# Kernel optimization log

Measured on AMD Instinct MI355X. Metric: run time of the kernel, lower is better.

## Reference

```python
import jax, jax.numpy as jnp
import numpy as np

P = 16        # patch size
SIM = 0.3     # similarity threshold (forward default arg `sim`)
STY_STD = 1000.0


def patchify(imgs):
    # (N,3,H,W) -> (N, h*w, p*p*3)
    N, C, H, W = imgs.shape
    h, w = H // P, W // P
    x = imgs.reshape(N, C, h, P, w, P)
    x = jnp.einsum('nchpwq->nhwpqc', x)
    return x.reshape(N, h * w, P * P * C)


def setup_inputs() -> dict:
    key = jax.random.key(0)
    k1, k2, k3, k4 = jax.random.split(key, 4)
    N, L, D = 2, 196, 768
    x = jax.random.normal(k1, (N, L + 1, D), dtype=jnp.float32)
    imgs = jax.random.normal(k2, (N, 3, 224, 224), dtype=jnp.float32)
    # torch trunc_normal_(std=1000, a=-2, b=2) == truncated normal on [-2,2]
    learnable_sty = (jax.random.truncated_normal(
        k3, -2.0 / STY_STD, 2.0 / STY_STD, (N, L, L, 1), dtype=jnp.float32) * STY_STD)
    noise = jax.random.normal(k4, (N, L, L, 1), dtype=jnp.float32)
    return {"x": x, "imgs": imgs, "learnable_sty": learnable_sty, "noise": noise}


def reference(x, imgs, learnable_sty, noise):
    imgs = patchify(imgs)                                   # (N, L, 768)
    cls_tokens, x = x[:, :1], x[:, 1:]
    N, L, D = x.shape

    # per-patch normalization (torch.var default is unbiased -> ddof=1)
    mean = imgs.mean(axis=-1, keepdims=True)
    var = jnp.var(imgs, axis=-1, keepdims=True, ddof=1)
    imgs_n = (imgs - mean) / jnp.sqrt(var + 1e-6)
    nrm = jnp.linalg.norm(imgs_n, axis=-1)                  # (N, L)
    Sim = jnp.einsum('aik,ajk->aij', imgs_n, imgs_n) / (nrm[:, :, None] * nrm[:, None, :])

    M0 = jnp.triu((Sim > SIM).astype(jnp.float32))          # (N, L, L), binary
    rows = jnp.arange(L)

    def body(i, M):
        # original loop breaks when sum == N*L; we freeze M once that holds
        done = M.sum() == N * L
        mask = (M[:, i, :] == 0).astype(M.dtype)            # (N, L)
        # rows <= i unchanged (M*M == M for binary), rows > i masked
        upd = jnp.where(rows[None, :, None] > i, M * mask[:, None, :], M)
        return jnp.where(done, M, upd)

    M = jax.lax.fori_loop(0, L - 1, body, M0)

    # decompose: phase (con) keeps grad, amplitude (sty) is detached
    fft = jnp.fft.fftn(x, axes=(-1,))
    con, sty = jnp.angle(fft), jnp.abs(fft)
    sty_d = jax.lax.stop_gradient(sty)

    avg_sum = (M[..., None] * sty_d[:, None, :, :]).sum(axis=2)   # (N, L, D)
    sty_mask = (avg_sum > 0).astype(jnp.float32)                   # (N, L, D)
    num = M.sum(axis=2)[..., None]                                 # (N, L, 1)
    avg = avg_sum / jnp.clip(num, 1e-7, None)                      # (N, L, D)
    std = jnp.sqrt(
        (M[..., None] * (sty_d[:, None, :, :] - avg[:, :, None, :]) ** 2).sum(axis=2)
        / jnp.clip(num, 1e-7, None))                               # (N, L, D)

    sty_para = sty_mask[:, None, :, :] * learnable_sty             # (N, L, L, D)
    sty_para = sty_para / jnp.clip(sty_para.sum(axis=2, keepdims=True), 1e-7, None)
    various = noise * std[:, None, :, :] + avg[:, None, :, :]      # (N, L, L, D)
    sum_sty = (sty_para * various).sum(axis=2)                     # (N, L, D)

    # compose: ifft(amp * e^{i phase}), torch .float() keeps the real part
    out = jnp.real(jnp.fft.ifftn(sum_sty * jnp.exp(1j * con), axes=(-1,))).astype(jnp.float32)
    return jnp.concatenate((cls_tokens, out), axis=1)
```

## Files before the change

kernel.cpp:

```cpp
#include <hip/hip_runtime.h>
#include <math.h>

typedef unsigned long long u64;

#define NBATCH 2
#define LTOK 196
#define DDIM 768
#define NROWS (NBATCH*LTOK)
#define NLD (NBATCH*LTOK*DDIM)

#define PI_F 3.14159265358979323846f
#define S3 0.86602540378443864676f

__device__ __forceinline__ void fft_butterfly(float* re, float* im,
                                              const float2* T,
                                              int tau, int s, int half) {
  int sub = tau >> 7;
  int b = tau & 127;
  int j = b & (half - 1);
  int p0 = (sub << 8) + ((b >> (s - 1)) << s) + j;
  int p1 = p0 + half;
  float2 w = T[j << (8 - s)];
  float xr = re[p1], xi = im[p1];
  float tr = w.x * xr - w.y * xi;
  float ti = w.x * xi + w.y * xr;
  float ur = re[p0], ui = im[p0];
  re[p0] = ur + tr; im[p0] = ui + ti;
  re[p1] = ur - tr; im[p1] = ui - ti;
}

__device__ __forceinline__ void fft_stages(float* re, float* im,
                                           const float2* T, int t) {
#pragma unroll
  for (int s = 1; s <= 8; s++) {
    int half = 1 << (s - 1);
    fft_butterfly(re, im, T, t, s, half);
    if (t < 128) fft_butterfly(re, im, T, t + 256, s, half);
    __syncthreads();
  }
}

__global__ __launch_bounds__(256) void k_pre(const float* __restrict__ imgs,
                                             const float* __restrict__ x,
                                             float* __restrict__ uT,
                                             float* __restrict__ sty,
                                             float* __restrict__ phre,
                                             float* __restrict__ phim) {
  int t = threadIdx.x;
  if (blockIdx.x < NROWS) {
    int blk = blockIdx.x;
    int a = blk / LTOK, l = blk - a * LTOK;
    int hh = l / 14, ww = l - hh * 14;
    float loc[3];
    double s = 0.0, sq = 0.0;
#pragma unroll
    for (int e = 0; e < 3; e++) {
      int d = t + (e << 8);
      int p = d / 48, r = d - p * 48;
      int q2 = r / 3, c = r - q2 * 3;
      float val = imgs[((size_t)(a * 3 + c) * 224 + (hh * 16 + p)) * 224 + (ww * 16 + q2)];
      loc[e] = val;
      s += (double)val;
      sq += (double)val * (double)val;
    }
#pragma unroll
    for (int o = 32; o > 0; o >>= 1) { s += __shfl_down(s, o); sq += __shfl_down(sq, o); }
    __shared__ double rs[4], rq[4];
    __shared__ float sh_mu, sh_sc;
    if ((t & 63) == 0) { rs[t >> 6] = s; rq[t >> 6] = sq; }
    __syncthreads();
    if (t == 0) {
      double S = rs[0] + rs[1] + rs[2] + rs[3];
      double Q = rq[0] + rq[1] + rq[2] + rq[3];
      double mean = S / 768.0;
      double ss = Q - S * S / 768.0;
      if (ss < 1e-30) ss = 1e-30;
      sh_mu = (float)mean;
      sh_sc = (float)(1.0 / sqrt(ss));
    }
    __syncthreads();
    float mu = sh_mu, sc = sh_sc;
    int col = a * LTOK + l;
#pragma unroll
    for (int e = 0; e < 3; e++) {
      int d = t + (e << 8);
      uT[(size_t)d * NROWS + col] = (loc[e] - mu) * sc;
    }
  } else {
    int blk = blockIdx.x - NROWS;
    int a = blk / LTOK, i = blk - a * LTOK;
    __shared__ float re[768], im[768];
    __shared__ float2 t256[128];
    if (t < 128) {
      float sn, cs;
      __sincosf(-2.0f * PI_F * (float)t / 256.0f, &sn, &cs);
      t256[t] = make_float2(cs, sn);
    }
    size_t row = ((size_t)a * (LTOK + 1) + 1 + i) * DDIM;
#pragma unroll
    for (int e = 0; e < 3; e++) {
      int d = t + (e << 8);
      int m = d / 3, r = d - 3 * m;
      int p = (r << 8) + (__brev((unsigned)m) >> 24);
      re[p] = x[row + d];
      im[p] = 0.f;
    }
    __syncthreads();
    fft_stages(re, im, t256, t);
    float a0r = re[t],       a0i = im[t];
    float a1r = re[256 + t], a1i = im[256 + t];
    float a2r = re[512 + t], a2i = im[512 + t];
    float sn, cs;
    __sincosf(-2.0f * PI_F * (float)t / 768.0f, &sn, &cs);
    float2 w1 = make_float2(cs, sn);
    float2 w2 = make_float2(cs * cs - sn * sn, 2.f * cs * sn);
    float b1r = a1r * w1.x - a1i * w1.y, b1i = a1r * w1.y + a1i * w1.x;
    float b2r = a2r * w2.x - a2i * w2.y, b2i = a2r * w2.y + a2i * w2.x;
    float Xr[3], Xi[3];
    Xr[0] = a0r + b1r + b2r;
    Xi[0] = a0i + b1i + b2i;
    Xr[1] = a0r + (-0.5f * b1r + S3 * b1i) + (-0.5f * b2r - S3 * b2i);
    Xi[1] = a0i + (-0.5f * b1i - S3 * b1r) + (-0.5f * b2i + S3 * b2r);
    Xr[2] = a0r + (-0.5f * b1r - S3 * b1i) + (-0.5f * b2r + S3 * b2i);
    Xi[2] = a0i + (-0.5f * b1i + S3 * b1r) + (-0.5f * b2i - S3 * b2r);
    size_t ob = ((size_t)a * LTOK + i) * DDIM + t;
#pragma unroll
    for (int s = 0; s < 3; s++) {
      float mag = sqrtf(Xr[s] * Xr[s] + Xi[s] * Xi[s]);
      size_t o = ob + (s << 8);
      sty[o] = mag;
      if (mag > 0.f) { phre[o] = Xr[s] / mag; phim[o] = Xi[s] / mag; }
      else           { phre[o] = 1.f;         phim[o] = 0.f;         }
    }
  }
}

__global__ __launch_bounds__(256) void k_sim(const float* __restrict__ uT,
                                             u64* __restrict__ Mb) {
  int blk = blockIdx.x;
  int a = blk / LTOK, i = blk - a * LTOK;
  __shared__ float ui[768];
  __shared__ u64 mask[4];
  int t = threadIdx.x;
  if (t < 4) mask[t] = 0ull;
  int coli = a * LTOK + i;
#pragma unroll
  for (int e = 0; e < 3; e++) {
    int d = t + (e << 8);
    ui[d] = uT[(size_t)d * NROWS + coli];
  }
  __syncthreads();
  int j = i + t;
  if (j < LTOK) {
    const float* col = uT + (a * LTOK + j);
    float dot = 0.f;
#pragma unroll 8
    for (int d = 0; d < 768; d++) dot += ui[d] * col[(size_t)d * NROWS];
    if (dot > 0.3f) atomicOr(&mask[j >> 6], 1ull << (j & 63));
  }
  __syncthreads();
  if (t < 4) Mb[((size_t)a * LTOK + i) * 4 + t] = mask[t];
}

__global__ __launch_bounds__(256) void k_greedy(u64* __restrict__ Mb) {
  __shared__ u64 Ml[NROWS * 4];
  __shared__ int red[4];
  __shared__ int Sdone;
  int t = threadIdx.x;
  for (int w = t; w < NROWS * 4; w += 256) Ml[w] = Mb[w];
  __syncthreads();
  for (int i = 0; i < LTOK - 1; i++) {
    int s = 0;
    for (int w = t; w < NROWS * 4; w += 256) s += __popcll(Ml[w]);
#pragma unroll
    for (int o = 32; o > 0; o >>= 1) s += __shfl_down(s, o);
    if ((t & 63) == 0) red[t >> 6] = s;
    __syncthreads();
    if (t == 0) Sdone = ((red[0] + red[1] + red[2] + red[3]) == NROWS) ? 1 : 0;
    __syncthreads();
    if (Sdone) break;
    for (int w = t; w < NROWS * 4; w += 256) {
      int a = w / (LTOK * 4);
      int rem = w - a * (LTOK * 4);
      int r = rem >> 2, wi = rem & 3;
      if (r > i) Ml[w] &= ~Ml[(a * LTOK + i) * 4 + wi];
    }
    __syncthreads();
  }
  for (int w = t; w < NROWS * 4; w += 256) Mb[w] = Ml[w];
}

__global__ __launch_bounds__(256) void k_stats(const u64* __restrict__ Mb,
                                               const float* __restrict__ sty,
                                               float* __restrict__ savg,
                                               float* __restrict__ sstd,
                                               float* __restrict__ smsk) {
  int blk = blockIdx.x;
  int a = blk / LTOK, i = blk - a * LTOK;
  __shared__ u64 mrow[4];
  int t = threadIdx.x;
  if (t < 4) mrow[t] = Mb[((size_t)a * LTOK + i) * 4 + t];
  __syncthreads();
  int num = __popcll(mrow[0]) + __popcll(mrow[1]) + __popcll(mrow[2]) + __popcll(mrow[3]);
  float fnum = fmaxf((float)num, 1e-7f);
  float acc0 = 0.f, acc1 = 0.f, acc2 = 0.f;
  for (int w = 0; w < 4; w++) {
    u64 m = mrow[w];
    while (m) {
      int b = __ffsll(m) - 1; m &= (m - 1);
      int j = (w << 6) + b;
      const float* sr = sty + ((size_t)a * LTOK + j) * DDIM;
      acc0 += sr[t]; acc1 += sr[t + 256]; acc2 += sr[t + 512];
    }
  }
  float av0 = acc0 / fnum, av1 = acc1 / fnum, av2 = acc2 / fnum;
  float sq0 = 0.f, sq1 = 0.f, sq2 = 0.f;
  for (int w = 0; w < 4; w++) {
    u64 m = mrow[w];
    while (m) {
      int b = __ffsll(m) - 1; m &= (m - 1);
      int j = (w << 6) + b;
      const float* sr = sty + ((size_t)a * LTOK + j) * DDIM;
      float d0 = sr[t] - av0, d1 = sr[t + 256] - av1, d2 = sr[t + 512] - av2;
      sq0 += d0 * d0; sq1 += d1 * d1; sq2 += d2 * d2;
    }
  }
  size_t o = ((size_t)a * LTOK + i) * DDIM + t;
  float mk0 = acc0 > 0.f ? 1.f : 0.f;
  float mk1 = acc1 > 0.f ? 1.f : 0.f;
  float mk2 = acc2 > 0.f ? 1.f : 0.f;
  smsk[o] = mk0;            smsk[o + 256] = mk1;            smsk[o + 512] = mk2;
  savg[o] = mk0 * av0;      savg[o + 256] = mk1 * av1;      savg[o + 512] = mk2 * av2;
  sstd[o] = mk0 * sqrtf(sq0 / fnum);
  sstd[o + 256] = mk1 * sqrtf(sq1 / fnum);
  sstd[o + 512] = mk2 * sqrtf(sq2 / fnum);
}

#define RTILE 7
#define JCH 4
#define JLEN 49
__global__ __launch_bounds__(256) void k_combine_part(const float* __restrict__ ls,
                                                      const float* __restrict__ nz,
                                                      const float* __restrict__ savg,
                                                      const float* __restrict__ sstd,
                                                      const float* __restrict__ smsk,
                                                      float* __restrict__ numP,
                                                      float* __restrict__ denP) {
  int blk = blockIdx.x;
  int a = blk / 336;
  int rem = blk - a * 336;
  int it = rem / 12;
  int r2 = rem - it * 12;
  int dc = r2 >> 2;
  int jc = r2 & 3;
  int i0 = it * RTILE;
  int j0 = jc * JLEN;
  int t = threadIdx.x;
  int d = (dc << 8) + t;
  __shared__ float lsr[RTILE][JLEN], lnr[RTILE][JLEN];
  for (int idx = t; idx < RTILE * JLEN; idx += 256) {
    int ii = idx / JLEN, j = idx - ii * JLEN;
    size_t o = ((size_t)(a * LTOK + i0 + ii)) * LTOK + j0 + j;
    float l = ls[o];
    lsr[ii][j] = l;
    lnr[ii][j] = l * nz[o];
  }
  __syncthreads();
  float nm[RTILE], dn[RTILE];
#pragma unroll
  for (int ii = 0; ii < RTILE; ii++) { nm[ii] = 0.f; dn[ii] = 0.f; }
#pragma unroll 7
  for (int j = 0; j < JLEN; j++) {
    size_t b = ((size_t)(a * LTOK + j0 + j)) * DDIM + d;
    float sd = sstd[b], sv = savg[b], sm = smsk[b];
#pragma unroll
    for (int ii = 0; ii < RTILE; ii++) {
      nm[ii] += lnr[ii][j] * sd;
      nm[ii] += lsr[ii][j] * sv;
      dn[ii] += lsr[ii][j] * sm;
    }
  }
#pragma unroll
  for (int ii = 0; ii < RTILE; ii++) {
    size_t o = ((size_t)jc * NROWS + (a * LTOK + i0 + ii)) * DDIM + d;
    numP[o] = nm[ii];
    denP[o] = dn[ii];
  }
}

__global__ __launch_bounds__(256) void k_ifft(const float* __restrict__ x,
                                              const float* __restrict__ numP,
                                              const float* __restrict__ denP,
                                              const float* __restrict__ phre,
                                              const float* __restrict__ phim,
                                              float* __restrict__ out) {
  int blk = blockIdx.x;
  int t = threadIdx.x;
  if (blk < NBATCH) {
    size_t b = (size_t)blk * (LTOK + 1) * DDIM;
    out[b + t] = x[b + t];
    out[b + t + 256] = x[b + t + 256];
    out[b + t + 512] = x[b + t + 512];
    return;
  }
  int rr = blk - NBATCH;
  int a = rr / LTOK, i = rr - a * LTOK;
  __shared__ float re[768], im[768];
  __shared__ float2 t256[128];
  if (t < 128) {
    float sn, cs;
    __sincosf(2.0f * PI_F * (float)t / 256.0f, &sn, &cs);
    t256[t] = make_float2(cs, sn);
  }
  size_t rowz = ((size_t)a * LTOK + i) * DDIM;
#pragma unroll
  for (int e = 0; e < 3; e++) {
    int d = t + (e << 8);
    float num = 0.f, den = 0.f;
#pragma unroll
    for (int jc = 0; jc < JCH; jc++) {
      size_t o = (size_t)jc * NROWS * DDIM + rowz + d;
      num += numP[o];
      den += denP[o];
    }
    float mg = num / fmaxf(den, 1e-7f);
    int m = d / 3, r = d - 3 * m;
    int p = (r << 8) + (__brev((unsigned)m) >> 24);
    re[p] = mg * phre[rowz + d];
    im[p] = mg * phim[rowz + d];
  }
  __syncthreads();
  fft_stages(re, im, t256, t);
  float a0r = re[t],       a0i = im[t];
  float a1r = re[256 + t], a1i = im[256 + t];
  float a2r = re[512 + t], a2i = im[512 + t];
  float sn, cs;
  __sincosf(2.0f * PI_F * (float)t / 768.0f, &sn, &cs);
  float2 w1 = make_float2(cs, sn);
  float2 w2 = make_float2(cs * cs - sn * sn, 2.f * cs * sn);
  float b1r = a1r * w1.x - a1i * w1.y, b1i = a1r * w1.y + a1i * w1.x;
  float b2r = a2r * w2.x - a2i * w2.y, b2i = a2r * w2.y + a2i * w2.x;
  float Xr[3];
  Xr[0] = a0r + b1r + b2r;
  Xr[1] = a0r + (-0.5f * b1r - S3 * b1i) + (-0.5f * b2r + S3 * b2i);
  Xr[2] = a0r + (-0.5f * b1r + S3 * b1i) + (-0.5f * b2r - S3 * b2i);
  size_t ob = ((size_t)a * (LTOK + 1) + 1 + i) * DDIM + t;
  const float inv = 1.0f / 768.0f;
  out[ob]       = Xr[0] * inv;
  out[ob + 256] = Xr[1] * inv;
  out[ob + 512] = Xr[2] * inv;
}

extern "C" void kernel_launch(void* const* d_in, const int* in_sizes, int n_in,
                              void* d_out, int out_size, void* d_ws, size_t ws_size,
                              hipStream_t stream) {
  (void)in_sizes; (void)n_in; (void)out_size; (void)ws_size;
  const float* x    = (const float*)d_in[0];
  const float* imgs = (const float*)d_in[1];
  const float* ls   = (const float*)d_in[2];
  const float* nz   = (const float*)d_in[3];
  float* out = (float*)d_out;

  float* wf   = (float*)d_ws;
  float* uT   = wf;
  float* sty  = wf + (size_t)NLD;
  float* phre = wf + 2 * (size_t)NLD;
  float* phim = wf + 3 * (size_t)NLD;
  float* sstd = wf + 4 * (size_t)NLD;
  float* smsk = wf + 5 * (size_t)NLD;
  float* numP = wf + 6 * (size_t)NLD;
  float* denP = wf + 10 * (size_t)NLD;
  u64* Mb = (u64*)(wf + 14 * (size_t)NLD);

  k_pre         <<<2 * NROWS, 256, 0, stream>>>(imgs, x, uT, sty, phre, phim);
  k_sim         <<<NROWS, 256, 0, stream>>>(uT, Mb);
  k_greedy      <<<1, 256, 0, stream>>>(Mb);
  k_stats       <<<NROWS, 256, 0, stream>>>(Mb, sty, uT , sstd, smsk);
  k_combine_part<<<NBATCH * 28 * 3 * JCH, 256, 0, stream>>>(ls, nz, uT , sstd, smsk, numP, denP);
  k_ifft        <<<NBATCH + NROWS, 256, 0, stream>>>(x, numP, denP, phre, phim, out);
}
```

Before: 125.4 us.

## Fuse all stages into one cooperative persistent kernel with grid syncs

Replaces six separate kernel launches with a single cooperative kernel of 512 persistent blocks. Each stage loops over its tasks and is separated from the next by grid.sync(), with shared memory held in one union. The goal is to remove launch overhead and the gaps between kernels. In exchange the greedy stage runs on one block while the rest wait, grid barriers add cost, the combine tile grows from 7 to 14 rows, and occupancy is limited by the launch-bounds hint.

```diff
diff --git a/kernel.cpp b/kernel.cpp
--- a/kernel.cpp
+++ b/kernel.cpp
@@ -1,5 +1,8 @@
 #include <hip/hip_runtime.h>
+#include <hip/hip_cooperative_groups.h>
 #include <math.h>
+
+namespace cg = cooperative_groups;
 
 typedef unsigned long long u64;
 
@@ -8,9 +11,23 @@
 #define DDIM 768
 #define NROWS (NBATCH*LTOK)
 #define NLD (NBATCH*LTOK*DDIM)
+#define GRID 512
 
 #define PI_F 3.14159265358979323846f
 #define S3 0.86602540378443864676f
+
+#define RT 14
+#define JCH 4
+#define JLEN 49
+
+union SMem {
+  struct { float re[768]; float im[768]; float2 t256[128]; } fft;
+  struct { float ui[768]; u64 mask[4]; } sim;
+  struct { u64 Ml[NROWS * 4]; int red[4]; int done; } greedy;
+  struct { u64 mrow[4]; } stats;
+  struct { float lsr[RT][JLEN]; float lnr[RT][JLEN]; } comb;
+  struct { double rs[4], rq[4]; float mu, sc; } patch;
+};
 
 __device__ __forceinline__ void fft_butterfly(float* re, float* im,
                                               const float2* T,
@@ -40,315 +57,301 @@
   }
 }
 
-__global__ __launch_bounds__(256) void k_pre(const float* __restrict__ imgs,
-                                             const float* __restrict__ x,
-                                             float* __restrict__ uT,
-                                             float* __restrict__ sty,
-                                             float* __restrict__ phre,
-                                             float* __restrict__ phim) {
+__global__ __launch_bounds__(256, 2) void k_mono(const float* __restrict__ imgs,
+                                                 const float* __restrict__ x,
+                                                 const float* __restrict__ ls,
+                                                 const float* __restrict__ nz,
+                                                 float* __restrict__ out,
+                                                 float* __restrict__ uT,
+                                                 float* __restrict__ sty,
+                                                 float* __restrict__ phre,
+                                                 float* __restrict__ phim,
+                                                 float* __restrict__ sstd,
+                                                 float* __restrict__ smsk,
+                                                 float* __restrict__ numP,
+                                                 float* __restrict__ denP,
+                                                 u64* __restrict__ Mb) {
+  cg::grid_group grid = cg::this_grid();
+  __shared__ SMem sm;
   int t = threadIdx.x;
-  if (blockIdx.x < NROWS) {
-    int blk = blockIdx.x;
-    int a = blk / LTOK, l = blk - a * LTOK;
-    int hh = l / 14, ww = l - hh * 14;
-    float loc[3];
-    double s = 0.0, sq = 0.0;
+
+  for (int task = blockIdx.x; task < 2 * NROWS; task += GRID) {
+    if (task < NROWS) {
+      int a = task / LTOK, l = task - a * LTOK;
+      int hh = l / 14, ww = l - hh * 14;
+      float loc[3];
+      double s = 0.0, sq = 0.0;
+#pragma unroll
+      for (int e = 0; e < 3; e++) {
+        int d = t + (e << 8);
+        int p = d / 48, r = d - p * 48;
+        int q2 = r / 3, c = r - q2 * 3;
+        float val = imgs[((size_t)(a * 3 + c) * 224 + (hh * 16 + p)) * 224 + (ww * 16 + q2)];
+        loc[e] = val;
+        s += (double)val;
+        sq += (double)val * (double)val;
+      }
+#pragma unroll
+      for (int o = 32; o > 0; o >>= 1) { s += __shfl_down(s, o); sq += __shfl_down(sq, o); }
+      if ((t & 63) == 0) { sm.patch.rs[t >> 6] = s; sm.patch.rq[t >> 6] = sq; }
+      __syncthreads();
+      if (t == 0) {
+        double S = sm.patch.rs[0] + sm.patch.rs[1] + sm.patch.rs[2] + sm.patch.rs[3];
+        double Q = sm.patch.rq[0] + sm.patch.rq[1] + sm.patch.rq[2] + sm.patch.rq[3];
+        double mean = S / 768.0;
+        double ss = Q - S * S / 768.0;
+        if (ss < 1e-30) ss = 1e-30;
+        sm.patch.mu = (float)mean;
+        sm.patch.sc = (float)(1.0 / sqrt(ss));
+      }
+      __syncthreads();
+      float mu = sm.patch.mu, sc = sm.patch.sc;
+      int col = a * LTOK + l;
+#pragma unroll
+      for (int e = 0; e < 3; e++) {
+        int d = t + (e << 8);
+        uT[(size_t)d * NROWS + col] = (loc[e] - mu) * sc;
+      }
+    } else {
+      int blk = task - NROWS;
+      int a = blk / LTOK, i = blk - a * LTOK;
+      if (t < 128) {
+        float sn, cs;
+        __sincosf(-2.0f * PI_F * (float)t / 256.0f, &sn, &cs);
+        sm.fft.t256[t] = make_float2(cs, sn);
+      }
+      size_t row = ((size_t)a * (LTOK + 1) + 1 + i) * DDIM;
+#pragma unroll
+      for (int e = 0; e < 3; e++) {
+        int d = t + (e << 8);
+        int m = d / 3, r = d - 3 * m;
+        int p = (r << 8) + (__brev((unsigned)m) >> 24);
+        sm.fft.re[p] = x[row + d];
+        sm.fft.im[p] = 0.f;
+      }
+      __syncthreads();
+      fft_stages(sm.fft.re, sm.fft.im, sm.fft.t256, t);
+      float a0r = sm.fft.re[t],       a0i = sm.fft.im[t];
+      float a1r = sm.fft.re[256 + t], a1i = sm.fft.im[256 + t];
+      float a2r = sm.fft.re[512 + t], a2i = sm.fft.im[512 + t];
+      float sn, cs;
+      __sincosf(-2.0f * PI_F * (float)t / 768.0f, &sn, &cs);
+      float2 w1 = make_float2(cs, sn);
+      float2 w2 = make_float2(cs * cs - sn * sn, 2.f * cs * sn);
+      float b1r = a1r * w1.x - a1i * w1.y, b1i = a1r * w1.y + a1i * w1.x;
+      float b2r = a2r * w2.x - a2i * w2.y, b2i = a2r * w2.y + a2i * w2.x;
+      float Xr[3], Xi[3];
+      Xr[0] = a0r + b1r + b2r;
+      Xi[0] = a0i + b1i + b2i;
+      Xr[1] = a0r + (-0.5f * b1r + S3 * b1i) + (-0.5f * b2r - S3 * b2i);
+      Xi[1] = a0i + (-0.5f * b1i - S3 * b1r) + (-0.5f * b2i + S3 * b2r);
+      Xr[2] = a0r + (-0.5f * b1r - S3 * b1i) + (-0.5f * b2r + S3 * b2i);
+      Xi[2] = a0i + (-0.5f * b1i + S3 * b1r) + (-0.5f * b2i - S3 * b2r);
+      size_t ob = ((size_t)a * LTOK + i) * DDIM + t;
+#pragma unroll
+      for (int s = 0; s < 3; s++) {
+        float mag = sqrtf(Xr[s] * Xr[s] + Xi[s] * Xi[s]);
+        size_t o = ob + (s << 8);
+        sty[o] = mag;
+        if (mag > 0.f) { phre[o] = Xr[s] / mag; phim[o] = Xi[s] / mag; }
+        else           { phre[o] = 1.f;         phim[o] = 0.f;         }
+      }
+    }
+    __syncthreads();
+  }
+  grid.sync();
+
+  for (int task = blockIdx.x; task < NROWS; task += GRID) {
+    int a = task / LTOK, i = task - a * LTOK;
+    if (t < 4) sm.sim.mask[t] = 0ull;
+    int coli = a * LTOK + i;
 #pragma unroll
     for (int e = 0; e < 3; e++) {
       int d = t + (e << 8);
-      int p = d / 48, r = d - p * 48;
-      int q2 = r / 3, c = r - q2 * 3;
-      float val = imgs[((size_t)(a * 3 + c) * 224 + (hh * 16 + p)) * 224 + (ww * 16 + q2)];
-      loc[e] = val;
-      s += (double)val;
-      sq += (double)val * (double)val;
-    }
-#pragma unroll
-    for (int o = 32; o > 0; o >>= 1) { s += __shfl_down(s, o); sq += __shfl_down(sq, o); }
-    __shared__ double rs[4], rq[4];
-    __shared__ float sh_mu, sh_sc;
-    if ((t & 63) == 0) { rs[t >> 6] = s; rq[t >> 6] = sq; }
-    __syncthreads();
-    if (t == 0) {
-      double S = rs[0] + rs[1] + rs[2] + rs[3];
-      double Q = rq[0] + rq[1] + rq[2] + rq[3];
-      double mean = S / 768.0;
-      double ss = Q - S * S / 768.0;
-      if (ss < 1e-30) ss = 1e-30;
-      sh_mu = (float)mean;
-      sh_sc = (float)(1.0 / sqrt(ss));
-    }
-    __syncthreads();
-    float mu = sh_mu, sc = sh_sc;
-    int col = a * LTOK + l;
+      sm.sim.ui[d] = uT[(size_t)d * NROWS + coli];
+    }
+    __syncthreads();
+    int j = i + t;
+    if (j < LTOK) {
+      const float* col = uT + (a * LTOK + j);
+      float dot = 0.f;
+#pragma unroll 8
+      for (int d = 0; d < 768; d++) dot += sm.sim.ui[d] * col[(size_t)d * NROWS];
+      if (dot > 0.3f) atomicOr(&sm.sim.mask[j >> 6], 1ull << (j & 63));
+    }
+    __syncthreads();
+    if (t < 4) Mb[((size_t)a * LTOK + i) * 4 + t] = sm.sim.mask[t];
+    __syncthreads();
+  }
+  grid.sync();
+
+  if (blockIdx.x == 0) {
+    for (int w = t; w < NROWS * 4; w += 256) sm.greedy.Ml[w] = Mb[w];
+    __syncthreads();
+    for (int i = 0; i < LTOK - 1; i++) {
+      int s = 0;
+      for (int w = t; w < NROWS * 4; w += 256) s += __popcll(sm.greedy.Ml[w]);
+#pragma unroll
+      for (int o = 32; o > 0; o >>= 1) s += __shfl_down(s, o);
+      if ((t & 63) == 0) sm.greedy.red[t >> 6] = s;
+      __syncthreads();
+      if (t == 0)
+        sm.greedy.done = ((sm.greedy.red[0] + sm.greedy.red[1] +
+                           sm.greedy.red[2] + sm.greedy.red[3]) == NROWS) ? 1 : 0;
+      __syncthreads();
+      if (sm.greedy.done) break;
+      for (int w = t; w < NROWS * 4; w += 256) {
+        int a = w / (LTOK * 4);
+        int rem = w - a * (LTOK * 4);
+        int r = rem >> 2, wi = rem & 3;
+        if (r > i) sm.greedy.Ml[w] &= ~sm.greedy.Ml[(a * LTOK + i) * 4 + wi];
+      }
+      __syncthreads();
+    }
+    for (int w = t; w < NROWS * 4; w += 256) Mb[w] = sm.greedy.Ml[w];
+  }
+  grid.sync();
+
+  for (int task = blockIdx.x; task < NROWS; task += GRID) {
+    int a = task / LTOK, i = task - a * LTOK;
+    if (t < 4) sm.stats.mrow[t] = Mb[((size_t)a * LTOK + i) * 4 + t];
+    __syncthreads();
+    u64 m0 = sm.stats.mrow[0], m1 = sm.stats.mrow[1],
+        m2 = sm.stats.mrow[2], m3 = sm.stats.mrow[3];
+    int num = __popcll(m0) + __popcll(m1) + __popcll(m2) + __popcll(m3);
+    float fnum = fmaxf((float)num, 1e-7f);
+    float acc0 = 0.f, acc1 = 0.f, acc2 = 0.f;
+    u64 mr[4] = {m0, m1, m2, m3};
+    for (int w = 0; w < 4; w++) {
+      u64 m = mr[w];
+      while (m) {
+        int b = __ffsll(m) - 1; m &= (m - 1);
+        int j = (w << 6) + b;
+        const float* sr = sty + ((size_t)a * LTOK + j) * DDIM;
+        acc0 += sr[t]; acc1 += sr[t + 256]; acc2 += sr[t + 512];
+      }
+    }
+    float av0 = acc0 / fnum, av1 = acc1 / fnum, av2 = acc2 / fnum;
+    float sq0 = 0.f, sq1 = 0.f, sq2 = 0.f;
+    for (int w = 0; w < 4; w++) {
+      u64 m = mr[w];
+      while (m) {
+        int b = __ffsll(m) - 1; m &= (m - 1);
+        int j = (w << 6) + b;
+        const float* sr = sty + ((size_t)a * LTOK + j) * DDIM;
+        float d0 = sr[t] - av0, d1 = sr[t + 256] - av1, d2 = sr[t + 512] - av2;
+        sq0 += d0 * d0; sq1 += d1 * d1; sq2 += d2 * d2;
+      }
+    }
+    size_t o = ((size_t)a * LTOK + i) * DDIM + t;
+    float mk0 = acc0 > 0.f ? 1.f : 0.f;
+    float mk1 = acc1 > 0.f ? 1.f : 0.f;
+    float mk2 = acc2 > 0.f ? 1.f : 0.f;
+    smsk[o] = mk0;            smsk[o + 256] = mk1;            smsk[o + 512] = mk2;
+    uT[o] = mk0 * av0;        uT[o + 256] = mk1 * av1;        uT[o + 512] = mk2 * av2;
+    sstd[o] = mk0 * sqrtf(sq0 / fnum);
+    sstd[o + 256] = mk1 * sqrtf(sq1 / fnum);
+    sstd[o + 512] = mk2 * sqrtf(sq2 / fnum);
+  }
+  grid.sync();
+
+  for (int task = blockIdx.x; task < NBATCH * RT * 3 * JCH; task += GRID) {
+    int a = task / 168;
+    int rem = task - a * 168;
+    int it = rem / 12;
+    int r2 = rem - it * 12;
+    int dc = r2 >> 2;
+    int jc = r2 & 3;
+    int i0 = it * RT;
+    int j0 = jc * JLEN;
+    int d = (dc << 8) + t;
+    for (int idx = t; idx < RT * JLEN; idx += 256) {
+      int ii = idx / JLEN, j = idx - ii * JLEN;
+      size_t o = ((size_t)(a * LTOK + i0 + ii)) * LTOK + j0 + j;
+      float l = ls[o];
+      sm.comb.lsr[ii][j] = l;
+      sm.comb.lnr[ii][j] = l * nz[o];
+    }
+    __syncthreads();
+    float nm[RT], dn[RT];
+#pragma unroll
+    for (int ii = 0; ii < RT; ii++) { nm[ii] = 0.f; dn[ii] = 0.f; }
+#pragma unroll 7
+    for (int j = 0; j < JLEN; j++) {
+      size_t b = ((size_t)(a * LTOK + j0 + j)) * DDIM + d;
+      float sd = sstd[b], sv = uT[b], smv = smsk[b];
+#pragma unroll
+      for (int ii = 0; ii < RT; ii++) {
+        nm[ii] += sm.comb.lnr[ii][j] * sd;
+        nm[ii] += sm.comb.lsr[ii][j] * sv;
+        dn[ii] += sm.comb.lsr[ii][j] * smv;
+      }
+    }
+#pragma unroll
+    for (int ii = 0; ii < RT; ii++) {
+      size_t o = ((size_t)jc * NROWS + (a * LTOK + i0 + ii)) * DDIM + d;
+      numP[o] = nm[ii];
+      denP[o] = dn[ii];
+    }
+    __syncthreads();
+  }
+  grid.sync();
+
+  for (int task = blockIdx.x; task < NBATCH + NROWS; task += GRID) {
+    if (task < NBATCH) {
+      size_t b = (size_t)task * (LTOK + 1) * DDIM;
+      out[b + t] = x[b + t];
+      out[b + t + 256] = x[b + t + 256];
+      out[b + t + 512] = x[b + t + 512];
+      __syncthreads();
+      continue;
+    }
+    int rr = task - NBATCH;
+    int a = rr / LTOK, i = rr - a * LTOK;
+    if (t < 128) {
+      float sn, cs;
+      __sincosf(2.0f * PI_F * (float)t / 256.0f, &sn, &cs);
+      sm.fft.t256[t] = make_float2(cs, sn);
+    }
+    size_t rowz = ((size_t)a * LTOK + i) * DDIM;
 #pragma unroll
     for (int e = 0; e < 3; e++) {
       int d = t + (e << 8);
-      uT[(size_t)d * NROWS + col] = (loc[e] - mu) * sc;
-    }
-  } else {
-    int blk = blockIdx.x - NROWS;
-    int a = blk / LTOK, i = blk - a * LTOK;
-    __shared__ float re[768], im[768];
-    __shared__ float2 t256[128];
-    if (t < 128) {
-      float sn, cs;
-      __sincosf(-2.0f * PI_F * (float)t / 256.0f, &sn, &cs);
-      t256[t] = make_float2(cs, sn);
-    }
-    size_t row = ((size_t)a * (LTOK + 1) + 1 + i) * DDIM;
-#pragma unroll
-    for (int e = 0; e < 3; e++) {
-      int d = t + (e << 8);
+      float num = 0.f, den = 0.f;
+#pragma unroll
+      for (int jc = 0; jc < JCH; jc++) {
+        size_t o = (size_t)jc * NROWS * DDIM + rowz + d;
+        num += numP[o];
+        den += denP[o];
+      }
+      float mg = num / fmaxf(den, 1e-7f);
       int m = d / 3, r = d - 3 * m;
       int p = (r << 8) + (__brev((unsigned)m) >> 24);
-      re[p] = x[row + d];
-      im[p] = 0.f;
-    }
-    __syncthreads();
-    fft_stages(re, im, t256, t);
-    float a0r = re[t],       a0i = im[t];
-    float a1r = re[256 + t], a1i = im[256 + t];
-    float a2r = re[512 + t], a2i = im[512 + t];
+      sm.fft.re[p] = mg * phre[rowz + d];
+      sm.fft.im[p] = mg * phim[rowz + d];
+    }
+    __syncthreads();
+    fft_stages(sm.fft.re, sm.fft.im, sm.fft.t256, t);
+    float a0r = sm.fft.re[t],       a0i = sm.fft.im[t];
+    float a1r = sm.fft.re[256 + t], a1i = sm.fft.im[256 + t];
+    float a2r = sm.fft.re[512 + t], a2i = sm.fft.im[512 + t];
     float sn, cs;
-    __sincosf(-2.0f * PI_F * (float)t / 768.0f, &sn, &cs);
+    __sincosf(2.0f * PI_F * (float)t / 768.0f, &sn, &cs);
     float2 w1 = make_float2(cs, sn);
     float2 w2 = make_float2(cs * cs - sn * sn, 2.f * cs * sn);
     float b1r = a1r * w1.x - a1i * w1.y, b1i = a1r * w1.y + a1i * w1.x;
     float b2r = a2r * w2.x - a2i * w2.y, b2i = a2r * w2.y + a2i * w2.x;
-    float Xr[3], Xi[3];
+    float Xr[3];
     Xr[0] = a0r + b1r + b2r;
-    Xi[0] = a0i + b1i + b2i;
-    Xr[1] = a0r + (-0.5f * b1r + S3 * b1i) + (-0.5f * b2r - S3 * b2i);
-    Xi[1] = a0i + (-0.5f * b1i - S3 * b1r) + (-0.5f * b2i + S3 * b2r);
-    Xr[2] = a0r + (-0.5f * b1r - S3 * b1i) + (-0.5f * b2r + S3 * b2i);
-    Xi[2] = a0i + (-0.5f * b1i + S3 * b1r) + (-0.5f * b2i - S3 * b2r);
-    size_t ob = ((size_t)a * LTOK + i) * DDIM + t;
-#pragma unroll
-    for (int s = 0; s < 3; s++) {
-      float mag = sqrtf(Xr[s] * Xr[s] + Xi[s] * Xi[s]);
-      size_t o = ob + (s << 8);
-      sty[o] = mag;
-      if (mag > 0.f) { phre[o] = Xr[s] / mag; phim[o] = Xi[s] / mag; }
-      else           { phre[o] = 1.f;         phim[o] = 0.f;         }
-    }
-  }
-}
-
-__global__ __launch_bounds__(256) void k_sim(const float* __restrict__ uT,
-                                             u64* __restrict__ Mb) {
-  int blk = blockIdx.x;
-  int a = blk / LTOK, i = blk - a * LTOK;
-  __shared__ float ui[768];
-  __shared__ u64 mask[4];
-  int t = threadIdx.x;
-  if (t < 4) mask[t] = 0ull;
-  int coli = a * LTOK + i;
-#pragma unroll
-  for (int e = 0; e < 3; e++) {
-    int d = t + (e << 8);
-    ui[d] = uT[(size_t)d * NROWS + coli];
-  }
-  __syncthreads();
-  int j = i + t;
-  if (j < LTOK) {
-    const float* col = uT + (a * LTOK + j);
-    float dot = 0.f;
-#pragma unroll 8
-    for (int d = 0; d < 768; d++) dot += ui[d] * col[(size_t)d * NROWS];
-    if (dot > 0.3f) atomicOr(&mask[j >> 6], 1ull << (j & 63));
-  }
-  __syncthreads();
-  if (t < 4) Mb[((size_t)a * LTOK + i) * 4 + t] = mask[t];
-}
-
-__global__ __launch_bounds__(256) void k_greedy(u64* __restrict__ Mb) {
-  __shared__ u64 Ml[NROWS * 4];
-  __shared__ int red[4];
-  __shared__ int Sdone;
-  int t = threadIdx.x;
-  for (int w = t; w < NROWS * 4; w += 256) Ml[w] = Mb[w];
-  __syncthreads();
-  for (int i = 0; i < LTOK - 1; i++) {
-    int s = 0;
-    for (int w = t; w < NROWS * 4; w += 256) s += __popcll(Ml[w]);
-#pragma unroll
-    for (int o = 32; o > 0; o >>= 1) s += __shfl_down(s, o);
-    if ((t & 63) == 0) red[t >> 6] = s;
-    __syncthreads();
-    if (t == 0) Sdone = ((red[0] + red[1] + red[2] + red[3]) == NROWS) ? 1 : 0;
-    __syncthreads();
-    if (Sdone) break;
-    for (int w = t; w < NROWS * 4; w += 256) {
-      int a = w / (LTOK * 4);
-      int rem = w - a * (LTOK * 4);
-      int r = rem >> 2, wi = rem & 3;
-      if (r > i) Ml[w] &= ~Ml[(a * LTOK + i) * 4 + wi];
-    }
-    __syncthreads();
-  }
-  for (int w = t; w < NROWS * 4; w += 256) Mb[w] = Ml[w];
-}
-
-__global__ __launch_bounds__(256) void k_stats(const u64* __restrict__ Mb,
-                                               const float* __restrict__ sty,
-                                               float* __restrict__ savg,
-                                               float* __restrict__ sstd,
-                                               float* __restrict__ smsk) {
-  int blk = blockIdx.x;
-  int a = blk / LTOK, i = blk - a * LTOK;
-  __shared__ u64 mrow[4];
-  int t = threadIdx.x;
-  if (t < 4) mrow[t] = Mb[((size_t)a * LTOK + i) * 4 + t];
-  __syncthreads();
-  int num = __popcll(mrow[0]) + __popcll(mrow[1]) + __popcll(mrow[2]) + __popcll(mrow[3]);
-  float fnum = fmaxf((float)num, 1e-7f);
-  float acc0 = 0.f, acc1 = 0.f, acc2 = 0.f;
-  for (int w = 0; w < 4; w++) {
-    u64 m = mrow[w];
-    while (m) {
-      int b = __ffsll(m) - 1; m &= (m - 1);
-      int j = (w << 6) + b;
-      const float* sr = sty + ((size_t)a * LTOK + j) * DDIM;
-      acc0 += sr[t]; acc1 += sr[t + 256]; acc2 += sr[t + 512];
-    }
-  }
-  float av0 = acc0 / fnum, av1 = acc1 / fnum, av2 = acc2 / fnum;
-  float sq0 = 0.f, sq1 = 0.f, sq2 = 0.f;
-  for (int w = 0; w < 4; w++) {
-    u64 m = mrow[w];
-    while (m) {
-      int b = __ffsll(m) - 1; m &= (m - 1);
-      int j = (w << 6) + b;
-      const float* sr = sty + ((size_t)a * LTOK + j) * DDIM;
-      float d0 = sr[t] - av0, d1 = sr[t + 256] - av1, d2 = sr[t + 512] - av2;
-      sq0 += d0 * d0; sq1 += d1 * d1; sq2 += d2 * d2;
-    }
-  }
-  size_t o = ((size_t)a * LTOK + i) * DDIM + t;
-  float mk0 = acc0 > 0.f ? 1.f : 0.f;
-  float mk1 = acc1 > 0.f ? 1.f : 0.f;
-  float mk2 = acc2 > 0.f ? 1.f : 0.f;
-  smsk[o] = mk0;            smsk[o + 256] = mk1;            smsk[o + 512] = mk2;
-  savg[o] = mk0 * av0;      savg[o + 256] = mk1 * av1;      savg[o + 512] = mk2 * av2;
-  sstd[o] = mk0 * sqrtf(sq0 / fnum);
-  sstd[o + 256] = mk1 * sqrtf(sq1 / fnum);
-  sstd[o + 512] = mk2 * sqrtf(sq2 / fnum);
-}
-
-#define RTILE 7
-#define JCH 4
-#define JLEN 49
-__global__ __launch_bounds__(256) void k_combine_part(const float* __restrict__ ls,
-                                                      const float* __restrict__ nz,
-                                                      const float* __restrict__ savg,
-                                                      const float* __restrict__ sstd,
-                                                      const float* __restrict__ smsk,
-                                                      float* __restrict__ numP,
-                                                      float* __restrict__ denP) {
-  int blk = blockIdx.x;
-  int a = blk / 336;
-  int rem = blk - a * 336;
-  int it = rem / 12;
-  int r2 = rem - it * 12;
-  int dc = r2 >> 2;
-  int jc = r2 & 3;
-  int i0 = it * RTILE;
-  int j0 = jc * JLEN;
-  int t = threadIdx.x;
-  int d = (dc << 8) + t;
-  __shared__ float lsr[RTILE][JLEN], lnr[RTILE][JLEN];
-  for (int idx = t; idx < RTILE * JLEN; idx += 256) {
-    int ii = idx / JLEN, j = idx - ii * JLEN;
-    size_t o = ((size_t)(a * LTOK + i0 + ii)) * LTOK + j0 + j;
-    float l = ls[o];
-    lsr[ii][j] = l;
-    lnr[ii][j] = l * nz[o];
-  }
-  __syncthreads();
-  float nm[RTILE], dn[RTILE];
-#pragma unroll
-  for (int ii = 0; ii < RTILE; ii++) { nm[ii] = 0.f; dn[ii] = 0.f; }
-#pragma unroll 7
-  for (int j = 0; j < JLEN; j++) {
-    size_t b = ((size_t)(a * LTOK + j0 + j)) * DDIM + d;
-    float sd = sstd[b], sv = savg[b], sm = smsk[b];
-#pragma unroll
-    for (int ii = 0; ii < RTILE; ii++) {
-      nm[ii] += lnr[ii][j] * sd;
-      nm[ii] += lsr[ii][j] * sv;
-      dn[ii] += lsr[ii][j] * sm;
-    }
-  }
-#pragma unroll
-  for (int ii = 0; ii < RTILE; ii++) {
-    size_t o = ((size_t)jc * NROWS + (a * LTOK + i0 + ii)) * DDIM + d;
-    numP[o] = nm[ii];
-    denP[o] = dn[ii];
-  }
-}
-
-__global__ __launch_bounds__(256) void k_ifft(const float* __restrict__ x,
-                                              const float* __restrict__ numP,
-                                              const float* __restrict__ denP,
-                                              const float* __restrict__ phre,
-                                              const float* __restrict__ phim,
-                                              float* __restrict__ out) {
-  int blk = blockIdx.x;
-  int t = threadIdx.x;
-  if (blk < NBATCH) {
-    size_t b = (size_t)blk * (LTOK + 1) * DDIM;
-    out[b + t] = x[b + t];
-    out[b + t + 256] = x[b + t + 256];
-    out[b + t + 512] = x[b + t + 512];
-    return;
-  }
-  int rr = blk - NBATCH;
-  int a = rr / LTOK, i = rr - a * LTOK;
-  __shared__ float re[768], im[768];
-  __shared__ float2 t256[128];
-  if (t < 128) {
-    float sn, cs;
-    __sincosf(2.0f * PI_F * (float)t / 256.0f, &sn, &cs);
-    t256[t] = make_float2(cs, sn);
-  }
-  size_t rowz = ((size_t)a * LTOK + i) * DDIM;
-#pragma unroll
-  for (int e = 0; e < 3; e++) {
-    int d = t + (e << 8);
-    float num = 0.f, den = 0.f;
-#pragma unroll
-    for (int jc = 0; jc < JCH; jc++) {
-      size_t o = (size_t)jc * NROWS * DDIM + rowz + d;
-      num += numP[o];
-      den += denP[o];
-    }
-    float mg = num / fmaxf(den, 1e-7f);
-    int m = d / 3, r = d - 3 * m;
-    int p = (r << 8) + (__brev((unsigned)m) >> 24);
-    re[p] = mg * phre[rowz + d];
-    im[p] = mg * phim[rowz + d];
-  }
-  __syncthreads();
-  fft_stages(re, im, t256, t);
-  float a0r = re[t],       a0i = im[t];
-  float a1r = re[256 + t], a1i = im[256 + t];
-  float a2r = re[512 + t], a2i = im[512 + t];
-  float sn, cs;
-  __sincosf(2.0f * PI_F * (float)t / 768.0f, &sn, &cs);
-  float2 w1 = make_float2(cs, sn);
-  float2 w2 = make_float2(cs * cs - sn * sn, 2.f * cs * sn);
-  float b1r = a1r * w1.x - a1i * w1.y, b1i = a1r * w1.y + a1i * w1.x;
-  float b2r = a2r * w2.x - a2i * w2.y, b2i = a2r * w2.y + a2i * w2.x;
-  float Xr[3];
-  Xr[0] = a0r + b1r + b2r;
-  Xr[1] = a0r + (-0.5f * b1r - S3 * b1i) + (-0.5f * b2r + S3 * b2i);
-  Xr[2] = a0r + (-0.5f * b1r + S3 * b1i) + (-0.5f * b2r - S3 * b2i);
-  size_t ob = ((size_t)a * (LTOK + 1) + 1 + i) * DDIM + t;
-  const float inv = 1.0f / 768.0f;
-  out[ob]       = Xr[0] * inv;
-  out[ob + 256] = Xr[1] * inv;
-  out[ob + 512] = Xr[2] * inv;
+    Xr[1] = a0r + (-0.5f * b1r - S3 * b1i) + (-0.5f * b2r + S3 * b2i);
+    Xr[2] = a0r + (-0.5f * b1r + S3 * b1i) + (-0.5f * b2r - S3 * b2i);
+    size_t ob = ((size_t)a * (LTOK + 1) + 1 + i) * DDIM + t;
+    const float inv = 1.0f / 768.0f;
+    out[ob]       = Xr[0] * inv;
+    out[ob + 256] = Xr[1] * inv;
+    out[ob + 512] = Xr[2] * inv;
+    __syncthreads();
+  }
 }
 
 extern "C" void kernel_launch(void* const* d_in, const int* in_sizes, int n_in,
@@ -372,10 +375,10 @@
   float* denP = wf + 10 * (size_t)NLD;
   u64* Mb = (u64*)(wf + 14 * (size_t)NLD);
 
-  k_pre         <<<2 * NROWS, 256, 0, stream>>>(imgs, x, uT, sty, phre, phim);
-  k_sim         <<<NROWS, 256, 0, stream>>>(uT, Mb);
-  k_greedy      <<<1, 256, 0, stream>>>(Mb);
-  k_stats       <<<NROWS, 256, 0, stream>>>(Mb, sty, uT , sstd, smsk);
-  k_combine_part<<<NBATCH * 28 * 3 * JCH, 256, 0, stream>>>(ls, nz, uT , sstd, smsk, numP, denP);
-  k_ifft        <<<NBATCH + NROWS, 256, 0, stream>>>(x, numP, denP, phre, phim, out);
+  void* args[] = { (void*)&imgs, (void*)&x, (void*)&ls, (void*)&nz, (void*)&out,
+                   (void*)&uT, (void*)&sty, (void*)&phre, (void*)&phim,
+                   (void*)&sstd, (void*)&smsk, (void*)&numP, (void*)&denP,
+                   (void*)&Mb };
+  hipLaunchCooperativeKernel((const void*)k_mono, dim3(GRID), dim3(256),
+                             args, 0, stream);
 }
```

Result: slower. 435.8 us (+247.5%).
